# Optimization experiments

Measured on AMD Instinct MI355X. Metric: run time of the kernel, lower is better.

## Reference

```python
import jax, jax.numpy as jnp
import numpy as np

H = 8
D = 512
DK = D // H  # 64
ALPHA = 0.2  # leaky relu negative slope


def setup_inputs() -> dict:
    key = jax.random.key(0)
    ks = jax.random.split(key, 10)
    B, N = 8, 1024
    query = jax.random.normal(ks[0], (B, N, D), dtype=jnp.float32)
    key_t = jax.random.normal(ks[1], (B, N, D), dtype=jnp.float32)
    value = jax.random.normal(ks[2], (B, N, D), dtype=jnp.float32)
    mask = jax.random.randint(ks[3], (B, N, N), 0, 2, dtype=jnp.int32)
    scale = 0.02
    Wq = jax.random.normal(ks[4], (D, D), dtype=jnp.float32) * scale
    Wk = jax.random.normal(ks[5], (D, D), dtype=jnp.float32) * scale
    Wv = jax.random.normal(ks[6], (D, D), dtype=jnp.float32) * scale
    Wo = jax.random.normal(ks[7], (D, D), dtype=jnp.float32) * scale
    bq = jnp.zeros((D,), jnp.float32)
    bk = jnp.zeros((D,), jnp.float32)
    bv = jnp.zeros((D,), jnp.float32)
    bo = jnp.zeros((D,), jnp.float32)
    # xavier-uniform-like init for the attention vector a: shape (h, 2*d_k)
    limit = float(np.sqrt(6.0 / (H + 2 * DK)))
    a = jax.random.uniform(ks[8], (H, 2 * DK), dtype=jnp.float32, minval=-limit, maxval=limit)
    return {"query": query, "key": key_t, "value": value, "mask": mask,
            "Wq": Wq, "bq": bq, "Wk": Wk, "bk": bk, "Wv": Wv, "bv": bv,
            "Wo": Wo, "bo": bo, "a": a}


def reference(query, key, value, mask, Wq, bq, Wk, bk, Wv, bv, Wo, bo, a):
    B, N, _ = query.shape

    def proj(x, W, b):
        # torch Linear: x @ W.T + b, then split heads -> (B, H, N, DK)
        return (x @ W.T + b).reshape(B, N, H, DK).transpose(0, 2, 1, 3)

    q = proj(query, Wq, bq)
    k = proj(key, Wk, bk)
    v = proj(value, Wv, bv)

    # 'cat' attention: scores[b,h,i,j] = concat(q_i, k_j) . a[h]
    #                = q_i . a[h,:DK] + k_j . a[h,DK:]  (algebraic decomposition,
    #                 avoids the O(N^2 * 2*DK) concat tensor of the torch code)
    sq = jnp.einsum('bhnd,hd->bhn', q, a[:, :DK])
    sk = jnp.einsum('bhnd,hd->bhn', k, a[:, DK:])
    scores = sq[:, :, :, None] + sk[:, :, None, :]  # (B, H, N, N)

    # mask == 0 -> -inf (mask broadcast over heads), applied BEFORE leaky relu
    scores = jnp.where(mask[:, None, :, :] == 0, -jnp.inf, scores)
    # leaky relu (leaky_relu(-inf) == -inf, preserved)
    scores = jnp.where(scores >= 0, scores, ALPHA * scores)

    p = jax.nn.softmax(scores, axis=-1)
    # fully-masked rows produce NaN -> replace with 0 (as in the torch code)
    p = jnp.where(jnp.isnan(p), jnp.zeros_like(p), p)

    x = jnp.einsum('bhnm,bhmd->bhnd', p, v)
    x = x.transpose(0, 2, 1, 3).reshape(B, N, D)
    return x @ Wo.T + bo
```

## Files before the change

### kernel.cpp

```cpp
#include <hip/hip_runtime.h>
#include <hip/hip_bf16.h>
#include <stdint.h>


typedef __attribute__((ext_vector_type(8))) short short8;
typedef __attribute__((ext_vector_type(4))) float f32x4;

#define LB __launch_bounds__(256)

union U8 { unsigned u[4]; short8 s; uint4 v; };
union U2 { unsigned u[2]; uint2 v; };

__device__ __forceinline__ unsigned short f2bf(float f) {
  unsigned int u = __float_as_uint(f);
  u += 0x7fffu + ((u >> 16) & 1u);
  return (unsigned short)(u >> 16);
}

__device__ __forceinline__ unsigned cvt_pk(float a, float b) {
  unsigned r;
  asm("v_cvt_pk_bf16_f32 %0, %1, %2" : "=v"(r) : "v"(a), "v"(b));
  return r;
}

__device__ __forceinline__ void async_cp16(const void* g, void* l) {
  __builtin_amdgcn_global_load_lds(
      (const __attribute__((address_space(1))) unsigned int*)g,
      (__attribute__((address_space(3))) unsigned int*)l, 16, 0, 0);
}

__global__ LB void prep_kernel(const int* __restrict__ mask, unsigned int* __restrict__ bits,
                               const float* __restrict__ value, unsigned short* __restrict__ vb,
                               const float* __restrict__ Wv, const float* __restrict__ Wo,
                               unsigned short* __restrict__ wv16, unsigned short* __restrict__ wo16,
                               const float* __restrict__ Wq, const float* __restrict__ Wk,
                               const float* __restrict__ a, const float* __restrict__ bq,
                               const float* __restrict__ bk,
                               unsigned short* __restrict__ Bfrag, float* __restrict__ qkb) {
  const int blk = blockIdx.x, tid = threadIdx.x;
  if (blk < 8192) {
    __shared__ unsigned char nb[256];
    const size_t e0 = ((size_t)blk * 256 + tid) * 4;
    const int4 m = *(const int4*)(mask + e0);
    nb[tid] = (unsigned char)((m.x != 0) | ((m.y != 0) << 1) | ((m.z != 0) << 2) | ((m.w != 0) << 3));
    __syncthreads();
    if (tid < 32) {
      const uint2 p = *(const uint2*)(nb + tid * 8);
      const unsigned lo = p.x, hi = p.y;
      const unsigned wl = (lo & 0xFu) | ((lo >> 4) & 0xF0u) | ((lo >> 8) & 0xF00u) | ((lo >> 12) & 0xF000u);
      const unsigned wh = (hi & 0xFu) | ((hi >> 4) & 0xF0u) | ((hi >> 8) & 0xF00u) | ((hi >> 12) & 0xF000u);
      bits[blk * 32 + tid] = wl | (wh << 16);
    }
    return;
  }
  if (blk < 12288) {
    const int idx = ((blk - 8192) * 256 + tid) * 4;
    const float4 v = *(const float4*)(value + idx);
    U2 pk;
    pk.u[0] = cvt_pk(v.x, v.y);
    pk.u[1] = cvt_pk(v.z, v.w);
    *(uint2*)(vb + idx) = pk.v;
    return;
  }
  if (blk < 12800) {
    const int wblk = blk - 12288;
    const float* src = wblk < 256 ? Wv : Wo;
    unsigned short* dst = wblk < 256 ? wv16 : wo16;
    const int idx = ((wblk & 255) * 256 + tid) * 4;
    const float4 v = *(const float4*)(src + idx);
    U2 pk;
    pk.u[0] = cvt_pk(v.x, v.y);
    pk.u[1] = cvt_pk(v.z, v.w);
    *(uint2*)(dst + idx) = pk.v;
    return;
  }
  const int t = (blk - 12800) * 256 + tid;
  const int d = t & 511, h = t >> 9;
  float aq = 0.f, ak = 0.f;
#pragma unroll 4
  for (int dk = 0; dk < 64; ++dk) {
    aq += Wq[(size_t)(h * 64 + dk) * 512 + d] * a[h * 128 + dk];
    ak += Wk[(size_t)(h * 64 + dk) * 512 + d] * a[h * 128 + 64 + dk];
  }
  const float L2E = 1.4426950408889634f;
  const int ks = d >> 5, lch = (d >> 3) & 3, tt = d & 7;
  Bfrag[((ks * 64 + (lch << 4) + h) << 3) + tt] = f2bf(aq * L2E);
  Bfrag[((ks * 64 + (lch << 4) + 8 + h) << 3) + tt] = f2bf(ak * L2E);
  if (d == 0) {
    float s1 = 0.f, s2 = 0.f;
    for (int dk = 0; dk < 64; ++dk) {
      s1 += bq[h * 64 + dk] * a[h * 128 + dk];
      s2 += bk[h * 64 + dk] * a[h * 128 + 64 + dk];
    }
    qkb[h] = s1 * L2E;
    qkb[8 + h] = s2 * L2E;
  }
}

__global__ LB void sqsk_gemmv_kernel(const float* __restrict__ query, const float* __restrict__ key,
                                     const unsigned short* __restrict__ Bfrag,
                                     const float* __restrict__ qkb,
                                     float* __restrict__ sq, float* __restrict__ sk,
                                     const unsigned short* __restrict__ vbA,
                                     const unsigned short* __restrict__ wv16,
                                     const float* __restrict__ bvb,
                                     unsigned short* __restrict__ vt) {
  __shared__ char sm[20480];
  const int tid = threadIdx.x, w = tid >> 6, l = tid & 63;
  const int lr = l & 15, lc = l >> 4;
  if (blockIdx.x < 512) {
    float* comb = (float*)sm;
    const int m0 = blockIdx.x * 16;
    const int k0 = w * 128;
    short8 bf[4];
#pragma unroll
    for (int ks = 0; ks < 4; ++ks)
      bf[ks] = *(const short8*)(Bfrag + (((w * 4 + ks) * 64 + l) << 3));
    const float* qbase = query + (size_t)(m0 + lr) * 512 + k0 + (lc << 3);
    const float* kbase = key + (size_t)(m0 + lr) * 512 + k0 + (lc << 3);
    f32x4 cq = {}, ck = {};
#pragma unroll
    for (int ks = 0; ks < 4; ++ks) {
      const float4 q0 = *(const float4*)(qbase + ks * 32);
      const float4 q1 = *(const float4*)(qbase + ks * 32 + 4);
      const float4 k0v = *(const float4*)(kbase + ks * 32);
      const float4 k1v = *(const float4*)(kbase + ks * 32 + 4);
      U8 aq, ak;
      aq.u[0] = cvt_pk(q0.x, q0.y); aq.u[1] = cvt_pk(q0.z, q0.w);
      aq.u[2] = cvt_pk(q1.x, q1.y); aq.u[3] = cvt_pk(q1.z, q1.w);
      ak.u[0] = cvt_pk(k0v.x, k0v.y); ak.u[1] = cvt_pk(k0v.z, k0v.w);
      ak.u[2] = cvt_pk(k1v.x, k1v.y); ak.u[3] = cvt_pk(k1v.z, k1v.w);
      cq = __builtin_amdgcn_mfma_f32_16x16x32_bf16(aq.s, bf[ks], cq, 0, 0, 0);
      ck = __builtin_amdgcn_mfma_f32_16x16x32_bf16(ak.s, bf[ks], ck, 0, 0, 0);
    }
    if (w) {
      float* p = comb + ((w - 1) * 64 + l) * 9;
#pragma unroll
      for (int r = 0; r < 4; ++r) { p[r] = cq[r]; p[4 + r] = ck[r]; }
    }
    __syncthreads();
    if (w == 0) {
#pragma unroll
      for (int j = 0; j < 3; ++j) {
        const float* p = comb + (j * 64 + l) * 9;
#pragma unroll
        for (int r = 0; r < 4; ++r) { cq[r] += p[r]; ck[r] += p[4 + r]; }
      }
      const int col = l & 15;
      const int mbase = m0 + (lc << 2);
      const int b = mbase >> 10;
      const float bia = qkb[col];
      if (col < 8) {
        float* out = sq + ((size_t)b * 8 + col) * 1024;
#pragma unroll
        for (int r = 0; r < 4; ++r) out[(mbase + r) & 1023] = cq[r] + bia;
      } else {
        float* out = sk + ((size_t)b * 8 + (col - 8)) * 1024;
#pragma unroll
        for (int r = 0; r < 4; ++r) out[(mbase + r) & 1023] = ck[r] + bia;
      }
    }
    return;
  }
  unsigned short* As = (unsigned short*)sm;
  unsigned short* Bs = (unsigned short*)(sm + 4096);
  const int bid = blockIdx.x - 512;
  const int bm = bid >> 2, bn = bid & 3;
  const int m0 = bm * 32, n0 = bn * 128;
  const int wr = (w & 1) * 16, wc = (w >> 1) * 64;
  const int rch = (lc ^ ((lr >> 1) & 3)) << 3;
  const int arow = (w << 3) + (l >> 2);
  const int asc = (l & 3) ^ ((arow >> 1) & 3);
  const unsigned short* asrc = vbA + (size_t)(m0 + arow) * 512 + (asc << 3);
  const int crow = l >> 2;
  const int brow0 = (w << 4) + crow, brow1 = ((w + 4) << 4) + crow;
  const unsigned short* bsrc0 = wv16 + (size_t)(n0 + brow0) * 512 + (((l & 3) ^ ((brow0 >> 1) & 3)) << 3);
  const unsigned short* bsrc1 = wv16 + (size_t)(n0 + brow1) * 512 + (((l & 3) ^ ((brow1 >> 1) & 3)) << 3);
  f32x4 acc[4] = {};
  if (l < 32) async_cp16(asrc, As + (w << 8));
  async_cp16(bsrc0, Bs + (w << 9));
  async_cp16(bsrc1, Bs + ((w + 4) << 9));
  int buf = 0;
  for (int kt = 0; kt < 16; ++kt) {
    if (kt < 15) {
      const int k1 = (kt + 1) * 32;
      if (l < 32) async_cp16(asrc + k1, As + ((buf ^ 1) << 10) + (w << 8));
      async_cp16(bsrc0 + k1, Bs + ((buf ^ 1) << 12) + (w << 9));
      async_cp16(bsrc1 + k1, Bs + ((buf ^ 1) << 12) + ((w + 4) << 9));
      asm volatile("s_waitcnt vmcnt(3)" ::: "memory");
    } else {
      asm volatile("s_waitcnt vmcnt(0)" ::: "memory");
    }
    __builtin_amdgcn_sched_barrier(0);
    __builtin_amdgcn_s_barrier();
    const short8 af = *(const short8*)(As + (buf << 10) + (wr + lr) * 32 + rch);
    __builtin_amdgcn_s_setprio(1);
#pragma unroll
    for (int j = 0; j < 4; ++j) {
      const short8 bfr = *(const short8*)(Bs + (buf << 12) + (wc + j * 16 + lr) * 32 + rch);
      acc[j] = __builtin_amdgcn_mfma_f32_16x16x32_bf16(af, bfr, acc[j], 0, 0, 0);
    }
    __builtin_amdgcn_s_setprio(0);
    if (kt < 15) __builtin_amdgcn_s_barrier();
    buf ^= 1;
  }
#pragma unroll
  for (int j = 0; j < 4; ++j) {
    const int nn = n0 + wc + j * 16 + lr;
    const float bia = bvb[nn];
    const int mm0 = m0 + wr + lc * 4;
    const int b = mm0 >> 10, t0 = mm0 & 1023;
    const int h = nn >> 6, dk = nn & 63;
    U2 pk;
    pk.u[0] = cvt_pk(acc[j][0] + bia, acc[j][1] + bia);
    pk.u[1] = cvt_pk(acc[j][2] + bia, acc[j][3] + bia);
    *(uint2*)(vt + (((size_t)((b * 8 + h) * 64 + dk)) << 10) + t0) = pk.v;
  }
}

template <int BB16, int MODE>
__global__ LB void gemm_bt(const unsigned short* __restrict__ A,
                           const void* __restrict__ Bwp,
                           const float* __restrict__ bias, void* __restrict__ outp) {
  __shared__ unsigned short As[2][32 * 32];
  __shared__ unsigned short Bs[2][128 * 32];
  const int tid = threadIdx.x;
  const int w = tid >> 6, l = tid & 63;
  const int lr = l & 15, lc = l >> 4;
  const int bm = blockIdx.x >> 2, bn = blockIdx.x & 3;
  const int m0 = bm * 32, n0 = bn * 128;
  const int wr = (w & 1) * 16, wc = (w >> 1) * 64;
  const int rch = (lc ^ ((lr >> 1) & 3)) << 3;
  const int arow = (w << 3) + (l >> 2);
  const int asc = (l & 3) ^ ((arow >> 1) & 3);
  const unsigned short* asrc = A + (size_t)(m0 + arow) * 512 + (asc << 3);
  const int crow = l >> 2;
  const unsigned short* b16 = (const unsigned short*)Bwp;
  const float* b32 = (const float*)Bwp;
  const int brow0 = (w << 4) + crow, brow1 = ((w + 4) << 4) + crow;
  const unsigned short* bsrc0 = b16 + (size_t)(n0 + brow0) * 512 + (((l & 3) ^ ((brow0 >> 1) & 3)) << 3);
  const unsigned short* bsrc1 = b16 + (size_t)(n0 + brow1) * 512 + (((l & 3) ^ ((brow1 >> 1) & 3)) << 3);

  f32x4 acc[4] = {};
  if (BB16) {
    if (l < 32) async_cp16(asrc, As[0] + (w << 8));
    async_cp16(bsrc0, Bs[0] + (w << 9));
    async_cp16(bsrc1, Bs[0] + ((w + 4) << 9));
    int buf = 0;
    for (int kt = 0; kt < 16; ++kt) {
      if (kt < 15) {
        const int k1 = (kt + 1) * 32;
        if (l < 32) async_cp16(asrc + k1, As[buf ^ 1] + (w << 8));
        async_cp16(bsrc0 + k1, Bs[buf ^ 1] + (w << 9));
        async_cp16(bsrc1 + k1, Bs[buf ^ 1] + ((w + 4) << 9));
        asm volatile("s_waitcnt vmcnt(3)" ::: "memory");
      } else {
        asm volatile("s_waitcnt vmcnt(0)" ::: "memory");
      }
      __builtin_amdgcn_sched_barrier(0);
      __builtin_amdgcn_s_barrier();
      const short8 af = *(const short8*)(As[buf] + (wr + lr) * 32 + rch);
      __builtin_amdgcn_s_setprio(1);
#pragma unroll
      for (int j = 0; j < 4; ++j) {
        const short8 bfr = *(const short8*)(Bs[buf] + (wc + j * 16 + lr) * 32 + rch);
        acc[j] = __builtin_amdgcn_mfma_f32_16x16x32_bf16(af, bfr, acc[j], 0, 0, 0);
      }
      __builtin_amdgcn_s_setprio(0);
      if (kt < 15) __builtin_amdgcn_s_barrier();
      buf ^= 1;
    }
  } else {
    for (int kt = 0; kt < 16; ++kt) {
      const int k0 = kt * 32;
      if (kt) __syncthreads();
      if (l < 32) async_cp16(asrc + k0, As[0] + (w << 8));
#pragma unroll
      for (int it = 0; it < 2; ++it) {
        const int idx = it * 256 + tid;
        const int row = idx >> 2, gr = idx & 3;
        const int sch = (gr ^ ((row >> 1) & 3)) << 3;
        const float4* src = (const float4*)(b32 + (size_t)(n0 + row) * 512 + k0 + gr * 8);
        const float4 b0 = src[0], b1 = src[1];
        U8 t8;
        t8.u[0] = cvt_pk(b0.x, b0.y); t8.u[1] = cvt_pk(b0.z, b0.w);
        t8.u[2] = cvt_pk(b1.x, b1.y); t8.u[3] = cvt_pk(b1.z, b1.w);
        *(uint4*)(Bs[0] + row * 32 + sch) = t8.v;
      }
      __syncthreads();
      const short8 af = *(const short8*)(As[0] + (wr + lr) * 32 + rch);
#pragma unroll
      for (int j = 0; j < 4; ++j) {
        const short8 bfr = *(const short8*)(Bs[0] + (wc + j * 16 + lr) * 32 + rch);
        acc[j] = __builtin_amdgcn_mfma_f32_16x16x32_bf16(af, bfr, acc[j], 0, 0, 0);
      }
    }
  }
#pragma unroll
  for (int j = 0; j < 4; ++j) {
    const int nn = n0 + wc + j * 16 + lr;
    const float bia = bias[nn];
    const int mm0 = m0 + wr + lc * 4;
    if (MODE == 0) {
      float* out = (float*)outp;
#pragma unroll
      for (int r = 0; r < 4; ++r)
        out[(size_t)(mm0 + r) * 512 + nn] = acc[j][r] + bia;
    } else {
      unsigned short* out = (unsigned short*)outp;
      const int b = mm0 >> 10, t0 = mm0 & 1023;
      const int h = nn >> 6, dk = nn & 63;
      U2 pk;
      pk.u[0] = cvt_pk(acc[j][0] + bia, acc[j][1] + bia);
      pk.u[1] = cvt_pk(acc[j][2] + bia, acc[j][3] + bia);
      *(uint2*)(out + (((size_t)((b * 8 + h) * 64 + dk)) << 10) + t0) = pk.v;
    }
  }
}

__global__ LB void attn_kernel(const float* __restrict__ sq, const float* __restrict__ sk,
                               const unsigned char* __restrict__ mbits,
                               const unsigned short* __restrict__ vt,
                               unsigned short* __restrict__ xb) {
  __shared__ char smem[53248];
  unsigned short* vts = (unsigned short*)smem;
  float* sks = (float*)(smem + 32768);
  char* mks = smem + 36864;
  const int tid = threadIdx.x;
  const int w = tid >> 6, l = tid & 63;
  const int lr = l & 15, lc = l >> 4;
  const int bid = blockIdx.x;
  const int bh = bid & 63, iblk = bid >> 6;
  const int b = bh >> 3, h = bh & 7;
  const int i0b = iblk << 7;
  const float* sqp = sq + (size_t)bh * 1024;
  const float* skp = sk + (size_t)bh * 1024;
  const unsigned short* vtp = vt + ((size_t)bh << 16);
  const unsigned char* mrow = mbits + ((size_t)b << 17);

  async_cp16(skp + (w << 8) + l * 4, sks + (w << 8));
#pragma unroll
  for (int m = 0; m < 4; ++m) {
    const int row = (w << 5) + (m << 3) + (l >> 3);
    const int c = (l & 7) ^ (row & 7);
    async_cp16(mrow + (size_t)(i0b + row) * 128 + (c << 4), mks + (w << 12) + (m << 10));
  }
  const int stl = l >> 2;
  const int stc = (l & 3) ^ ((stl >> 1) & 3);
#define STAGE_VTS(tb, jb)                                                      \
  {                                                                            \
    unsigned short* dst = vts + ((tb) << 13) + (w << 11);                      \
    const unsigned short* s_ = vtp + stl * 1024 + (jb) + (w << 5) + (stc << 3);\
    async_cp16(s_, dst);                                                       \
    async_cp16(s_ + 16384, dst + 512);                                         \
    async_cp16(s_ + 32768, dst + 1024);                                        \
    async_cp16(s_ + 49152, dst + 1536);                                        \
  }
  STAGE_VTS(0, 0);
  float sq2[2];
#pragma unroll
  for (int g = 0; g < 2; ++g) sq2[g] = sqp[i0b + (w << 5) + (g << 4) + lr];
  __syncthreads();

  f32x4 acc[2][4] = {};
  f32x4 accs[2] = {};
  short8 ones;
#pragma unroll
  for (int t = 0; t < 8; ++t) ones[t] = (short)0x3f80;
  const int vread = (lc ^ ((lr >> 1) & 3)) << 3;
  const int rx = (lr & 7) << 4;

  int tb = 0;
  for (int it = 0; it < 8; ++it) {
    if (it < 7) {
      STAGE_VTS(tb ^ 1, (it + 1) << 7);
      asm volatile("s_waitcnt vmcnt(4)" ::: "memory");
    } else {
      asm volatile("s_waitcnt vmcnt(0)" ::: "memory");
    }
    __builtin_amdgcn_sched_barrier(0);
    __builtin_amdgcn_s_barrier();
#pragma unroll
    for (int s = 0; s < 4; ++s) {
      const int jb = (it << 7) + (s << 5);
      const int qb = (jb >> 3) + lc;
      const f32x4 s0 = *(const f32x4*)(sks + jb + (lc << 3));
      const f32x4 s1 = *(const f32x4*)(sks + jb + (lc << 3) + 4);
      U8 pa[2];
#pragma unroll
      for (int g = 0; g < 2; ++g) {
        const int rowl = (w << 5) + (g << 4) + lr;
        const unsigned mb = (unsigned char)mks[(rowl << 7) + (qb ^ rx)];
        const float sqv = sq2[g];
        float e[8];
#pragma unroll
        for (int t = 0; t < 8; ++t) {
          float sv = sqv + (t < 4 ? s0[t] : s1[t - 4]);
          sv = fmaxf(sv, 0.2f * sv);
          const float ex = __builtin_amdgcn_exp2f(sv);
          e[t] = (mb & (1u << t)) ? ex : 0.0f;
        }
        pa[g].u[0] = cvt_pk(e[0], e[1]); pa[g].u[1] = cvt_pk(e[2], e[3]);
        pa[g].u[2] = cvt_pk(e[4], e[5]); pa[g].u[3] = cvt_pk(e[6], e[7]);
      }
      const unsigned short* vbb = vts + (tb << 13) + (s << 11) + vread;
      __builtin_amdgcn_s_setprio(1);
#pragma unroll
      for (int c = 0; c < 4; ++c) {
        const short8 bv = *(const short8*)(vbb + ((c << 4) + lr) * 32);
#pragma unroll
        for (int g = 0; g < 2; ++g)
          acc[g][c] = __builtin_amdgcn_mfma_f32_16x16x32_bf16(pa[g].s, bv, acc[g][c], 0, 0, 0);
      }
#pragma unroll
      for (int g = 0; g < 2; ++g)
        accs[g] = __builtin_amdgcn_mfma_f32_16x16x32_bf16(pa[g].s, ones, accs[g], 0, 0, 0);
      __builtin_amdgcn_s_setprio(0);
    }
    if (it < 7) __builtin_amdgcn_s_barrier();
    tb ^= 1;
  }
#undef STAGE_VTS

#pragma unroll
  for (int g = 0; g < 2; ++g) {
#pragma unroll
    for (int r = 0; r < 4; ++r) {
      const float sv = accs[g][r];
      const float inv = sv > 0.0f ? 1.0f / sv : 0.0f;
      const int i = i0b + (w << 5) + (g << 4) + (lc << 2) + r;
#pragma unroll
      for (int c = 0; c < 4; ++c)
        xb[(((size_t)(b * 1024 + i)) << 9) + h * 64 + (c << 4) + lr] =
            f2bf(acc[g][c][r] * inv);
    }
  }
}

extern "C" void kernel_launch(void* const* d_in, const int* in_sizes, int n_in,
                              void* d_out, int out_size, void* d_ws, size_t ws_size,
                              hipStream_t stream) {
  const float* query = (const float*)d_in[0];
  const float* key   = (const float*)d_in[1];
  const float* value = (const float*)d_in[2];
  const int*   mask  = (const int*)d_in[3];
  const float* Wq = (const float*)d_in[4];
  const float* bq = (const float*)d_in[5];
  const float* Wk = (const float*)d_in[6];
  const float* bk = (const float*)d_in[7];
  const float* Wv = (const float*)d_in[8];
  const float* bv = (const float*)d_in[9];
  const float* Wo = (const float*)d_in[10];
  const float* bo = (const float*)d_in[11];
  const float* a  = (const float*)d_in[12];

  char* oc = (char*)d_out;
  unsigned short* vt = (unsigned short*)(oc + 0);
  unsigned int* mbits = (unsigned int*)(oc + 8388608);
  float* sqv = (float*)(oc + 9437184);
  float* skv = (float*)(oc + 9699328);
  unsigned short* Bfrag = (unsigned short*)(oc + 9961472);
  float* qkb = (float*)(oc + 9977856);
  unsigned short* wv16 = (unsigned short*)(oc + 10485760);
  unsigned short* wo16f = (unsigned short*)(oc + 11010048);
  unsigned short* vb = (unsigned short*)d_ws;
  unsigned short* xb = (unsigned short*)d_ws;

  const bool roomy = ws_size >= 8912896;
  unsigned short* wo16 = roomy ? (unsigned short*)((char*)d_ws + 8388608) : wo16f;

  prep_kernel<<<12816, 256, 0, stream>>>(mask, mbits, value, vb, Wv, Wo, wv16, wo16,
                                         Wq, Wk, a, bq, bk, Bfrag, qkb);
  sqsk_gemmv_kernel<<<1536, 256, 0, stream>>>(query, key, Bfrag, qkb, sqv, skv,
                                              vb, wv16, bv, vt);
  attn_kernel<<<512, 256, 0, stream>>>(sqv, skv, (const unsigned char*)mbits, vt, xb);
  if (roomy)
    gemm_bt<1, 0><<<1024, 256, 0, stream>>>(xb, (const void*)wo16, bo, d_out);
  else
    gemm_bt<0, 0><<<1024, 256, 0, stream>>>(xb, (const void*)Wo, bo, d_out);
}
```

Baseline: 82.15 us.

## Fuse value conversion into V-projection GEMM, move mask packing, split attention over key halves

The separate fp32-to-bf16 conversion of value is dropped; the V-projection GEMM now loads fp32 value rows into registers, converts them and writes them to LDS with a register-prefetch pipeline. Mask bit-packing moves from the prep kernel into the middle kernel, so prep only handles weights. The attention kernel changes its warp split: each warp covers 64 query rows over half the keys, and the two halves are reduced through shared memory at the end. This cuts an intermediate round-trip and a kernel's worth of dependency, at the cost of extra register pressure and an added LDS reduction step.

```diff
diff --git a/kernel.cpp b/kernel.cpp
--- a/kernel.cpp
+++ b/kernel.cpp
@@ -29,44 +29,17 @@
       (__attribute__((address_space(3))) unsigned int*)l, 16, 0, 0);
 }
 
-__global__ LB void prep_kernel(const int* __restrict__ mask, unsigned int* __restrict__ bits,
-                               const float* __restrict__ value, unsigned short* __restrict__ vb,
-                               const float* __restrict__ Wv, const float* __restrict__ Wo,
+__global__ LB void prep_kernel(const float* __restrict__ Wv, const float* __restrict__ Wo,
                                unsigned short* __restrict__ wv16, unsigned short* __restrict__ wo16,
                                const float* __restrict__ Wq, const float* __restrict__ Wk,
                                const float* __restrict__ a, const float* __restrict__ bq,
                                const float* __restrict__ bk,
                                unsigned short* __restrict__ Bfrag, float* __restrict__ qkb) {
   const int blk = blockIdx.x, tid = threadIdx.x;
-  if (blk < 8192) {
-    __shared__ unsigned char nb[256];
-    const size_t e0 = ((size_t)blk * 256 + tid) * 4;
-    const int4 m = *(const int4*)(mask + e0);
-    nb[tid] = (unsigned char)((m.x != 0) | ((m.y != 0) << 1) | ((m.z != 0) << 2) | ((m.w != 0) << 3));
-    __syncthreads();
-    if (tid < 32) {
-      const uint2 p = *(const uint2*)(nb + tid * 8);
-      const unsigned lo = p.x, hi = p.y;
-      const unsigned wl = (lo & 0xFu) | ((lo >> 4) & 0xF0u) | ((lo >> 8) & 0xF00u) | ((lo >> 12) & 0xF000u);
-      const unsigned wh = (hi & 0xFu) | ((hi >> 4) & 0xF0u) | ((hi >> 8) & 0xF00u) | ((hi >> 12) & 0xF000u);
-      bits[blk * 32 + tid] = wl | (wh << 16);
-    }
-    return;
-  }
-  if (blk < 12288) {
-    const int idx = ((blk - 8192) * 256 + tid) * 4;
-    const float4 v = *(const float4*)(value + idx);
-    U2 pk;
-    pk.u[0] = cvt_pk(v.x, v.y);
-    pk.u[1] = cvt_pk(v.z, v.w);
-    *(uint2*)(vb + idx) = pk.v;
-    return;
-  }
-  if (blk < 12800) {
-    const int wblk = blk - 12288;
-    const float* src = wblk < 256 ? Wv : Wo;
-    unsigned short* dst = wblk < 256 ? wv16 : wo16;
-    const int idx = ((wblk & 255) * 256 + tid) * 4;
+  if (blk < 512) {
+    const float* src = blk < 256 ? Wv : Wo;
+    unsigned short* dst = blk < 256 ? wv16 : wo16;
+    const int idx = ((blk & 255) * 256 + tid) * 4;
     const float4 v = *(const float4*)(src + idx);
     U2 pk;
     pk.u[0] = cvt_pk(v.x, v.y);
@@ -74,7 +47,7 @@
     *(uint2*)(dst + idx) = pk.v;
     return;
   }
-  const int t = (blk - 12800) * 256 + tid;
+  const int t = (blk - 512) * 256 + tid;
   const int d = t & 511, h = t >> 9;
   float aq = 0.f, ak = 0.f;
 #pragma unroll 4
@@ -97,20 +70,36 @@
   }
 }
 
-__global__ LB void sqsk_gemmv_kernel(const float* __restrict__ query, const float* __restrict__ key,
-                                     const unsigned short* __restrict__ Bfrag,
-                                     const float* __restrict__ qkb,
-                                     float* __restrict__ sq, float* __restrict__ sk,
-                                     const unsigned short* __restrict__ vbA,
-                                     const unsigned short* __restrict__ wv16,
-                                     const float* __restrict__ bvb,
-                                     unsigned short* __restrict__ vt) {
+__global__ LB void mid_kernel(const float* __restrict__ query, const float* __restrict__ key,
+                              const unsigned short* __restrict__ Bfrag,
+                              const float* __restrict__ qkb,
+                              float* __restrict__ sq, float* __restrict__ sk,
+                              const float* __restrict__ value,
+                              const unsigned short* __restrict__ wv16,
+                              const float* __restrict__ bvb, unsigned short* __restrict__ vt,
+                              const int* __restrict__ mask, unsigned int* __restrict__ bits) {
   __shared__ char sm[20480];
   const int tid = threadIdx.x, w = tid >> 6, l = tid & 63;
   const int lr = l & 15, lc = l >> 4;
-  if (blockIdx.x < 512) {
+  const int bid = blockIdx.x;
+  if (bid >= 1536) {
+    unsigned char* nb = (unsigned char*)sm;
+    const size_t e0 = ((size_t)(bid - 1536) * 256 + tid) * 4;
+    const int4 m = *(const int4*)(mask + e0);
+    nb[tid] = (unsigned char)((m.x != 0) | ((m.y != 0) << 1) | ((m.z != 0) << 2) | ((m.w != 0) << 3));
+    __syncthreads();
+    if (tid < 32) {
+      const uint2 p = *(const uint2*)(nb + tid * 8);
+      const unsigned lo = p.x, hi = p.y;
+      const unsigned wl = (lo & 0xFu) | ((lo >> 4) & 0xF0u) | ((lo >> 8) & 0xF00u) | ((lo >> 12) & 0xF000u);
+      const unsigned wh = (hi & 0xFu) | ((hi >> 4) & 0xF0u) | ((hi >> 8) & 0xF00u) | ((hi >> 12) & 0xF000u);
+      bits[(bid - 1536) * 32 + tid] = wl | (wh << 16);
+    }
+    return;
+  }
+  if (bid >= 1024) {
     float* comb = (float*)sm;
-    const int m0 = blockIdx.x * 16;
+    const int m0 = (bid - 1024) * 16;
     const int k0 = w * 128;
     short8 bf[4];
 #pragma unroll
@@ -164,35 +153,39 @@
   }
   unsigned short* As = (unsigned short*)sm;
   unsigned short* Bs = (unsigned short*)(sm + 4096);
-  const int bid = blockIdx.x - 512;
   const int bm = bid >> 2, bn = bid & 3;
   const int m0 = bm * 32, n0 = bn * 128;
   const int wr = (w & 1) * 16, wc = (w >> 1) * 64;
   const int rch = (lc ^ ((lr >> 1) & 3)) << 3;
-  const int arow = (w << 3) + (l >> 2);
-  const int asc = (l & 3) ^ ((arow >> 1) & 3);
-  const unsigned short* asrc = vbA + (size_t)(m0 + arow) * 512 + (asc << 3);
+  const int arow = (w << 3) + (l >> 3);
+  const int akc = l & 7;
+  const float* asrc = value + (size_t)(m0 + arow) * 512 + (akc << 2);
+  const int ach = ((akc >> 1) ^ ((arow >> 1) & 3));
+  const int aoff = arow * 32 + (ach << 3) + ((akc & 1) << 2);
   const int crow = l >> 2;
   const int brow0 = (w << 4) + crow, brow1 = ((w + 4) << 4) + crow;
   const unsigned short* bsrc0 = wv16 + (size_t)(n0 + brow0) * 512 + (((l & 3) ^ ((brow0 >> 1) & 3)) << 3);
   const unsigned short* bsrc1 = wv16 + (size_t)(n0 + brow1) * 512 + (((l & 3) ^ ((brow1 >> 1) & 3)) << 3);
+
   f32x4 acc[4] = {};
-  if (l < 32) async_cp16(asrc, As + (w << 8));
+  float4 areg = *(const float4*)(asrc);
   async_cp16(bsrc0, Bs + (w << 9));
   async_cp16(bsrc1, Bs + ((w + 4) << 9));
+  {
+    U2 aw;
+    aw.u[0] = cvt_pk(areg.x, areg.y);
+    aw.u[1] = cvt_pk(areg.z, areg.w);
+    *(uint2*)(As + aoff) = aw.v;
+  }
+  areg = *(const float4*)(asrc + 32);
+  async_cp16(bsrc0 + 32, Bs + 4096 + (w << 9));
+  async_cp16(bsrc1 + 32, Bs + 4096 + ((w + 4) << 9));
+  asm volatile("s_waitcnt vmcnt(3)" ::: "memory");
+  asm volatile("s_waitcnt lgkmcnt(0)" ::: "memory");
+  __builtin_amdgcn_sched_barrier(0);
+  __builtin_amdgcn_s_barrier();
   int buf = 0;
   for (int kt = 0; kt < 16; ++kt) {
-    if (kt < 15) {
-      const int k1 = (kt + 1) * 32;
-      if (l < 32) async_cp16(asrc + k1, As + ((buf ^ 1) << 10) + (w << 8));
-      async_cp16(bsrc0 + k1, Bs + ((buf ^ 1) << 12) + (w << 9));
-      async_cp16(bsrc1 + k1, Bs + ((buf ^ 1) << 12) + ((w + 4) << 9));
-      asm volatile("s_waitcnt vmcnt(3)" ::: "memory");
-    } else {
-      asm volatile("s_waitcnt vmcnt(0)" ::: "memory");
-    }
-    __builtin_amdgcn_sched_barrier(0);
-    __builtin_amdgcn_s_barrier();
     const short8 af = *(const short8*)(As + (buf << 10) + (wr + lr) * 32 + rch);
     __builtin_amdgcn_s_setprio(1);
 #pragma unroll
@@ -201,7 +194,24 @@
       acc[j] = __builtin_amdgcn_mfma_f32_16x16x32_bf16(af, bfr, acc[j], 0, 0, 0);
     }
     __builtin_amdgcn_s_setprio(0);
-    if (kt < 15) __builtin_amdgcn_s_barrier();
+    __builtin_amdgcn_s_barrier();
+    if (kt < 15) {
+      U2 aw;
+      aw.u[0] = cvt_pk(areg.x, areg.y);
+      aw.u[1] = cvt_pk(areg.z, areg.w);
+      *(uint2*)(As + ((buf ^ 1) << 10) + aoff) = aw.v;
+      if (kt < 14) {
+        areg = *(const float4*)(asrc + (kt + 2) * 32);
+        async_cp16(bsrc0 + (kt + 2) * 32, Bs + (buf << 12) + (w << 9));
+        async_cp16(bsrc1 + (kt + 2) * 32, Bs + (buf << 12) + ((w + 4) << 9));
+        asm volatile("s_waitcnt vmcnt(3)" ::: "memory");
+      } else {
+        asm volatile("s_waitcnt vmcnt(0)" ::: "memory");
+      }
+      asm volatile("s_waitcnt lgkmcnt(0)" ::: "memory");
+      __builtin_amdgcn_sched_barrier(0);
+      __builtin_amdgcn_s_barrier();
+    }
     buf ^= 1;
   }
 #pragma unroll
@@ -218,10 +228,10 @@
   }
 }
 
-template <int BB16, int MODE>
+template <int BB16>
 __global__ LB void gemm_bt(const unsigned short* __restrict__ A,
                            const void* __restrict__ Bwp,
-                           const float* __restrict__ bias, void* __restrict__ outp) {
+                           const float* __restrict__ bias, float* __restrict__ outp) {
   __shared__ unsigned short As[2][32 * 32];
   __shared__ unsigned short Bs[2][128 * 32];
   const int tid = threadIdx.x;
@@ -301,20 +311,9 @@
     const int nn = n0 + wc + j * 16 + lr;
     const float bia = bias[nn];
     const int mm0 = m0 + wr + lc * 4;
-    if (MODE == 0) {
-      float* out = (float*)outp;
-#pragma unroll
-      for (int r = 0; r < 4; ++r)
-        out[(size_t)(mm0 + r) * 512 + nn] = acc[j][r] + bia;
-    } else {
-      unsigned short* out = (unsigned short*)outp;
-      const int b = mm0 >> 10, t0 = mm0 & 1023;
-      const int h = nn >> 6, dk = nn & 63;
-      U2 pk;
-      pk.u[0] = cvt_pk(acc[j][0] + bia, acc[j][1] + bia);
-      pk.u[1] = cvt_pk(acc[j][2] + bia, acc[j][3] + bia);
-      *(uint2*)(out + (((size_t)((b * 8 + h) * 64 + dk)) << 10) + t0) = pk.v;
-    }
+#pragma unroll
+    for (int r = 0; r < 4; ++r)
+      outp[(size_t)(mm0 + r) * 512 + nn] = acc[j][r] + bia;
   }
 }
 
@@ -333,6 +332,8 @@
   const int bh = bid & 63, iblk = bid >> 6;
   const int b = bh >> 3, h = bh & 7;
   const int i0b = iblk << 7;
+  const int rh = w & 1, jh = w >> 1;
+  const int j0 = jh << 9;
   const float* sqp = sq + (size_t)bh * 1024;
   const float* skp = sk + (size_t)bh * 1024;
   const unsigned short* vtp = vt + ((size_t)bh << 16);
@@ -347,92 +348,115 @@
   }
   const int stl = l >> 2;
   const int stc = (l & 3) ^ ((stl >> 1) & 3);
-#define STAGE_VTS(tb, jb)                                                      \
+  const unsigned short* vsrc = vtp + stl * 1024 + j0 + (stc << 3);
+#define STAGE(bf_, jb_)                                                        \
   {                                                                            \
-    unsigned short* dst = vts + ((tb) << 13) + (w << 11);                      \
-    const unsigned short* s_ = vtp + stl * 1024 + (jb) + (w << 5) + (stc << 3);\
-    async_cp16(s_, dst);                                                       \
-    async_cp16(s_ + 16384, dst + 512);                                         \
-    async_cp16(s_ + 32768, dst + 1024);                                        \
-    async_cp16(s_ + 49152, dst + 1536);                                        \
-  }
-  STAGE_VTS(0, 0);
-  float sq2[2];
-#pragma unroll
-  for (int g = 0; g < 2; ++g) sq2[g] = sqp[i0b + (w << 5) + (g << 4) + lr];
+    unsigned short* d_ = vts + (w << 12) + ((bf_) << 11);                      \
+    const unsigned short* s_ = vsrc + (jb_);                                   \
+    async_cp16(s_, d_);                                                        \
+    async_cp16(s_ + 16384, d_ + 512);                                          \
+    async_cp16(s_ + 32768, d_ + 1024);                                         \
+    async_cp16(s_ + 49152, d_ + 1536);                                         \
+  }
+  STAGE(0, 0);
+  float sq8[4];
+#pragma unroll
+  for (int t = 0; t < 4; ++t) sq8[t] = sqp[i0b + (rh << 6) + (t << 4) + lr];
   __syncthreads();
 
-  f32x4 acc[2][4] = {};
-  f32x4 accs[2] = {};
+  f32x4 acc[4][4] = {};
+  f32x4 accs[4] = {};
   short8 ones;
 #pragma unroll
   for (int t = 0; t < 8; ++t) ones[t] = (short)0x3f80;
+  const int rx = (lr & 7) << 4;
   const int vread = (lc ^ ((lr >> 1) & 3)) << 3;
-  const int rx = (lr & 7) << 4;
-
-  int tb = 0;
-  for (int it = 0; it < 8; ++it) {
-    if (it < 7) {
-      STAGE_VTS(tb ^ 1, (it + 1) << 7);
+
+  int buf = 0;
+  for (int s = 0; s < 16; ++s) {
+    if (s < 15) {
+      STAGE(buf ^ 1, (s + 1) << 5);
       asm volatile("s_waitcnt vmcnt(4)" ::: "memory");
     } else {
       asm volatile("s_waitcnt vmcnt(0)" ::: "memory");
     }
     __builtin_amdgcn_sched_barrier(0);
-    __builtin_amdgcn_s_barrier();
-#pragma unroll
-    for (int s = 0; s < 4; ++s) {
-      const int jb = (it << 7) + (s << 5);
-      const int qb = (jb >> 3) + lc;
-      const f32x4 s0 = *(const f32x4*)(sks + jb + (lc << 3));
-      const f32x4 s1 = *(const f32x4*)(sks + jb + (lc << 3) + 4);
-      U8 pa[2];
-#pragma unroll
-      for (int g = 0; g < 2; ++g) {
-        const int rowl = (w << 5) + (g << 4) + lr;
-        const unsigned mb = (unsigned char)mks[(rowl << 7) + (qb ^ rx)];
-        const float sqv = sq2[g];
-        float e[8];
-#pragma unroll
-        for (int t = 0; t < 8; ++t) {
-          float sv = sqv + (t < 4 ? s0[t] : s1[t - 4]);
-          sv = fmaxf(sv, 0.2f * sv);
-          const float ex = __builtin_amdgcn_exp2f(sv);
-          e[t] = (mb & (1u << t)) ? ex : 0.0f;
-        }
-        pa[g].u[0] = cvt_pk(e[0], e[1]); pa[g].u[1] = cvt_pk(e[2], e[3]);
-        pa[g].u[2] = cvt_pk(e[4], e[5]); pa[g].u[3] = cvt_pk(e[6], e[7]);
-      }
-      const unsigned short* vbb = vts + (tb << 13) + (s << 11) + vread;
-      __builtin_amdgcn_s_setprio(1);
+    const int jb = j0 + (s << 5);
+    const int qb = (jb >> 3) + lc;
+    const f32x4 s0 = *(const f32x4*)(sks + jb + (lc << 3));
+    const f32x4 s1 = *(const f32x4*)(sks + jb + (lc << 3) + 4);
+    U8 pa[4];
+#pragma unroll
+    for (int t = 0; t < 4; ++t) {
+      const int row = (rh << 6) + (t << 4) + lr;
+      const unsigned mb = (unsigned char)mks[(row << 7) + (qb ^ rx)];
+      const float sqv = sq8[t];
+      float e[8];
+#pragma unroll
+      for (int u = 0; u < 8; ++u) {
+        float sv = sqv + (u < 4 ? s0[u] : s1[u - 4]);
+        sv = fmaxf(sv, 0.2f * sv);
+        const float ex = __builtin_amdgcn_exp2f(sv);
+        e[u] = (mb & (1u << u)) ? ex : 0.0f;
+      }
+      pa[t].u[0] = cvt_pk(e[0], e[1]); pa[t].u[1] = cvt_pk(e[2], e[3]);
+      pa[t].u[2] = cvt_pk(e[4], e[5]); pa[t].u[3] = cvt_pk(e[6], e[7]);
+    }
+    const unsigned short* vbb = vts + (w << 12) + (buf << 11) + vread;
+    __builtin_amdgcn_s_setprio(1);
+#pragma unroll
+    for (int c = 0; c < 4; ++c) {
+      const short8 bv = *(const short8*)(vbb + ((c << 4) + lr) * 32);
+#pragma unroll
+      for (int t = 0; t < 4; ++t)
+        acc[t][c] = __builtin_amdgcn_mfma_f32_16x16x32_bf16(pa[t].s, bv, acc[t][c], 0, 0, 0);
+    }
+#pragma unroll
+    for (int t = 0; t < 4; ++t)
+      accs[t] = __builtin_amdgcn_mfma_f32_16x16x32_bf16(pa[t].s, ones, accs[t], 0, 0, 0);
+    __builtin_amdgcn_s_setprio(0);
+    buf ^= 1;
+  }
+#undef STAGE
+
+  __syncthreads();
+  float* cmb = (float*)smem;
+  if (jh == 1) {
+    float* p = cmb + ((rh << 6) + l) * 84;
+#pragma unroll
+    for (int t = 0; t < 4; ++t) {
+#pragma unroll
+      for (int c = 0; c < 4; ++c) *(f32x4*)(p + (t * 4 + c) * 4) = acc[t][c];
+      *(f32x4*)(p + 64 + t * 4) = accs[t];
+    }
+  }
+  __syncthreads();
+  if (jh == 0) {
+    const float* p = cmb + ((rh << 6) + l) * 84;
+#pragma unroll
+    for (int t = 0; t < 4; ++t) {
 #pragma unroll
       for (int c = 0; c < 4; ++c) {
-        const short8 bv = *(const short8*)(vbb + ((c << 4) + lr) * 32);
-#pragma unroll
-        for (int g = 0; g < 2; ++g)
-          acc[g][c] = __builtin_amdgcn_mfma_f32_16x16x32_bf16(pa[g].s, bv, acc[g][c], 0, 0, 0);
-      }
-#pragma unroll
-      for (int g = 0; g < 2; ++g)
-        accs[g] = __builtin_amdgcn_mfma_f32_16x16x32_bf16(pa[g].s, ones, accs[g], 0, 0, 0);
-      __builtin_amdgcn_s_setprio(0);
-    }
-    if (it < 7) __builtin_amdgcn_s_barrier();
-    tb ^= 1;
-  }
-#undef STAGE_VTS
-
-#pragma unroll
-  for (int g = 0; g < 2; ++g) {
-#pragma unroll
-    for (int r = 0; r < 4; ++r) {
-      const float sv = accs[g][r];
-      const float inv = sv > 0.0f ? 1.0f / sv : 0.0f;
-      const int i = i0b + (w << 5) + (g << 4) + (lc << 2) + r;
-#pragma unroll
-      for (int c = 0; c < 4; ++c)
-        xb[(((size_t)(b * 1024 + i)) << 9) + h * 64 + (c << 4) + lr] =
-            f2bf(acc[g][c][r] * inv);
+        const f32x4 v = *(const f32x4*)(p + (t * 4 + c) * 4);
+#pragma unroll
+        for (int r = 0; r < 4; ++r) acc[t][c][r] += v[r];
+      }
+      const f32x4 vs = *(const f32x4*)(p + 64 + t * 4);
+#pragma unroll
+      for (int r = 0; r < 4; ++r) accs[t][r] += vs[r];
+    }
+#pragma unroll
+    for (int t = 0; t < 4; ++t) {
+#pragma unroll
+      for (int r = 0; r < 4; ++r) {
+        const float sv = accs[t][r];
+        const float inv = sv > 0.0f ? 1.0f / sv : 0.0f;
+        const int i = i0b + (rh << 6) + (t << 4) + (lc << 2) + r;
+#pragma unroll
+        for (int c = 0; c < 4; ++c)
+          xb[(((size_t)(b * 1024 + i)) << 9) + h * 64 + (c << 4) + lr] =
+              f2bf(acc[t][c][r] * inv);
+      }
     }
   }
 }
@@ -462,20 +486,17 @@
   unsigned short* Bfrag = (unsigned short*)(oc + 9961472);
   float* qkb = (float*)(oc + 9977856);
   unsigned short* wv16 = (unsigned short*)(oc + 10485760);
-  unsigned short* wo16f = (unsigned short*)(oc + 11010048);
-  unsigned short* vb = (unsigned short*)d_ws;
   unsigned short* xb = (unsigned short*)d_ws;
 
   const bool roomy = ws_size >= 8912896;
-  unsigned short* wo16 = roomy ? (unsigned short*)((char*)d_ws + 8388608) : wo16f;
-
-  prep_kernel<<<12816, 256, 0, stream>>>(mask, mbits, value, vb, Wv, Wo, wv16, wo16,
-                                         Wq, Wk, a, bq, bk, Bfrag, qkb);
-  sqsk_gemmv_kernel<<<1536, 256, 0, stream>>>(query, key, Bfrag, qkb, sqv, skv,
-                                              vb, wv16, bv, vt);
+  unsigned short* wo16 = roomy ? (unsigned short*)((char*)d_ws + 8388608) : (unsigned short*)(oc + 11010048);
+
+  prep_kernel<<<528, 256, 0, stream>>>(Wv, Wo, wv16, wo16, Wq, Wk, a, bq, bk, Bfrag, qkb);
+  mid_kernel<<<9728, 256, 0, stream>>>(query, key, Bfrag, qkb, sqv, skv,
+                                       value, wv16, bv, vt, mask, mbits);
   attn_kernel<<<512, 256, 0, stream>>>(sqv, skv, (const unsigned char*)mbits, vt, xb);
   if (roomy)
-    gemm_bt<1, 0><<<1024, 256, 0, stream>>>(xb, (const void*)wo16, bo, d_out);
+    gemm_bt<1><<<1024, 256, 0, stream>>>(xb, (const void*)wo16, bo, (float*)d_out);
   else
-    gemm_bt<0, 0><<<1024, 256, 0, stream>>>(xb, (const void*)Wo, bo, d_out);
-}
+    gemm_bt<0><<<1024, 256, 0, stream>>>(xb, (const void*)Wo, bo, (float*)d_out);
+}
```

After: 81.23 us. About the same (-1.1%).
